# Kernel tuning notes

Measured on AMD Instinct MI355X. Metric: run time of the kernel, lower is better.

## Reference

```python
import jax, jax.numpy as jnp
import numpy as np

B, NS, NT = 4, 512, 512
D_IN, C1, R, C2 = 128, 64, 32, 32
E = 32768
STEPS = 10


def setup_inputs() -> dict:
    key = jax.random.key(0)
    ks = jax.random.split(key, 12)
    inp = {}
    inp['x_s'] = jax.random.normal(ks[0], (B * NS, D_IN), jnp.float32)
    inp['edge_index_s'] = jax.random.randint(ks[1], (2, E), 0, B * NS, jnp.int32)
    inp['edge_attr_s'] = jax.random.uniform(ks[2], (E,), jnp.float32)
    inp['batch_s'] = (jnp.arange(B * NS, dtype=jnp.int32) // NS)
    inp['x_t'] = jax.random.normal(ks[3], (B * NT, D_IN), jnp.float32)
    inp['edge_index_t'] = jax.random.randint(ks[4], (2, E), 0, B * NT, jnp.int32)
    inp['edge_attr_t'] = jax.random.uniform(ks[5], (E,), jnp.float32)
    inp['batch_t'] = (jnp.arange(B * NT, dtype=jnp.int32) // NT)
    inp['W1'] = jax.random.normal(ks[6], (D_IN, C1), jnp.float32) / np.float32(np.sqrt(D_IN))
    inp['W2'] = jax.random.normal(ks[7], (R, C2), jnp.float32) / np.float32(np.sqrt(R))
    inp['mw1'] = jax.random.normal(ks[8], (C2, C2), jnp.float32) / np.float32(np.sqrt(C2))
    inp['mb1'] = jnp.zeros((C2,), jnp.float32)
    inp['mw2'] = jax.random.normal(ks[9], (C2, 1), jnp.float32) / np.float32(np.sqrt(C2))
    inp['mb2'] = jnp.zeros((1,), jnp.float32)
    inp['r'] = jax.random.normal(ks[10], (STEPS, B, NS, R), jnp.float32)
    return inp


def psi(x, src, dst, ea, W, n):
    # simple message-passing GNN: edge-weighted neighbor aggregation + linear + ReLU
    m = jax.ops.segment_sum(x[src] * ea[:, None], dst, num_segments=n)
    return jax.nn.relu((x + m) @ W)


def reference(x_s, edge_index_s, edge_attr_s, batch_s, x_t, edge_index_t, edge_attr_t,
              batch_t, W1, W2, mw1, mb1, mw2, mb2, r):
    # Uniform graph sizes -> to_dense_batch is a reshape and all masks are True,
    # so masked_softmax reduces to plain softmax; batch_s/batch_t kept for interface fidelity.
    ss, ds = edge_index_s[0], edge_index_s[1]
    st, dt = edge_index_t[0], edge_index_t[1]
    h_s = psi(x_s, ss, ds, edge_attr_s, W1, B * NS).reshape(B, NS, C1)
    h_t = psi(x_t, st, dt, edge_attr_t, W1, B * NT).reshape(B, NT, C1)
    S_hat0 = jnp.einsum('bsc,btc->bst', h_s, h_t)  # [B, NS, NT]
    S_0 = jax.nn.softmax(S_hat0, axis=-1)

    def step(S_hat, r_i):
        S = jax.nn.softmax(S_hat, axis=-1)
        r_t = jnp.einsum('bst,bsr->btr', S, r_i)  # S^T @ r_s
        o_s = psi(r_i.reshape(B * NS, R), ss, ds, edge_attr_s, W2, B * NS).reshape(B, NS, C2)
        o_t = psi(r_t.reshape(B * NT, R), st, dt, edge_attr_t, W2, B * NT).reshape(B, NT, C2)
        Dm = o_s[:, :, None, :] - o_t[:, None, :, :]  # [B, NS, NT, C2] outer difference
        upd = (jax.nn.relu(Dm @ mw1 + mb1) @ mw2 + mb2)[..., 0]
        return S_hat + upd, None

    S_hat, _ = jax.lax.scan(step, S_hat0, r)
    S_L = jax.nn.softmax(S_hat, axis=-1)
    return (S_0, S_L)
```

## Files before the change

kernel.cpp:

```cpp
#include <hip/hip_runtime.h>


constexpr int kB = 4;
constexpr int kNS = 512;
constexpr int kNT = 512;
constexpr int kDin = 128;
constexpr int kC1 = 64;
constexpr int kR = 32;
constexpr int kC2 = 32;
constexpr int kE = 32768;
constexpr int kSteps = 10;
constexpr int kN = kB * kNS;
constexpr int kChunkStride = kR * kN;

__global__ void k_hist(const int* __restrict__ ei_s, const int* __restrict__ ei_t,
                       int* __restrict__ deg) {
  int g = blockIdx.y;
  const int* dst = (g ? ei_t : ei_s) + kE;
  int e = blockIdx.x * 256 + threadIdx.x;
  atomicAdd(&deg[g * kN + dst[e]], 1);
}

__global__ void k_scan(const int* __restrict__ deg, int* __restrict__ off,
                       int* __restrict__ cur) {
  int g = blockIdx.x;
  const int* d = deg + g * kN;
  int* o = off + g * (kN + 1);
  int* c = cur + g * kN;
  __shared__ int sums[256];
  int tid = threadIdx.x;
  int loc[8];
  int s = 0;
#pragma unroll
  for (int i = 0; i < 8; ++i) { loc[i] = d[tid * 8 + i]; s += loc[i]; }
  sums[tid] = s;
  __syncthreads();
  for (int st = 1; st < 256; st <<= 1) {
    int v = (tid >= st) ? sums[tid - st] : 0;
    __syncthreads();
    sums[tid] += v;
    __syncthreads();
  }
  int base = (tid > 0) ? sums[tid - 1] : 0;
#pragma unroll
  for (int i = 0; i < 8; ++i) {
    int idx = tid * 8 + i;
    o[idx] = base;
    c[idx] = base;
    base += loc[i];
  }
  if (tid == 255) o[kN] = base;
}

__global__ void k_scatter(const int* __restrict__ ei_s, const int* __restrict__ ei_t,
                          const float* __restrict__ ea_s, const float* __restrict__ ea_t,
                          int* __restrict__ cur, int* __restrict__ srcs,
                          float* __restrict__ eaw) {
  int g = blockIdx.y;
  const int* ei = g ? ei_t : ei_s;
  const float* ea = g ? ea_t : ea_s;
  int e = blockIdx.x * 256 + threadIdx.x;
  int d = ei[kE + e];
  int srcv = ei[e];
  int pos = atomicAdd(&cur[g * kN + d], 1);
  srcs[g * kE + pos] = srcv;
  eaw[g * kE + pos] = ea[e];
}

__global__ __launch_bounds__(128) void k_psi1(
    const float* __restrict__ x_s, const float* __restrict__ x_t,
    const int* __restrict__ srcs, const float* __restrict__ eaw,
    const int* __restrict__ off, const float* __restrict__ W1, float* __restrict__ h) {
  int g = blockIdx.y;
  const float* x = g ? x_t : x_s;
  const int* sr = srcs + g * kE;
  const float* ew = eaw + g * kE;
  const int* o = off + g * (kN + 1);
  float* ho = h + (size_t)g * kN * kC1;
  int n = blockIdx.x, f = threadIdx.x;
  __shared__ float y[kDin];
  int beg = o[n], end = o[n + 1];
  float m = 0.f;
  for (int idx = beg; idx < end; ++idx)
    m += x[(size_t)sr[idx] * kDin + f] * ew[idx];
  y[f] = x[(size_t)n * kDin + f] + m;
  __syncthreads();
  if (f < kC1) {
    float acc = 0.f;
#pragma unroll 16
    for (int k = 0; k < kDin; ++k) acc += y[k] * W1[k * kC1 + f];
    ho[(size_t)n * kC1 + f] = fmaxf(acc, 0.f);
  }
}

__global__ __launch_bounds__(256) void k_shat0(const float* __restrict__ h,
                                               float* __restrict__ Shat,
                                               float* __restrict__ pstatm,
                                               float* __restrict__ pstatl) {
  int b = blockIdx.z, s0 = blockIdx.y * 64, t0 = blockIdx.x * 64;
  const float* hs = h + (size_t)(b * kNS + s0) * kC1;
  const float* ht = h + (size_t)kN * kC1 + (size_t)(b * kNT + t0) * kC1;
  __shared__ float As[64 * 68];
  __shared__ float Bs[64 * 68];
  int tid = threadIdx.x;
#pragma unroll
  for (int k2 = 0; k2 < 4; ++k2) {
    int idx = tid + k2 * 256;
    int row = idx >> 4, c4 = idx & 15;
    float4 va = *(const float4*)(hs + (size_t)row * kC1 + c4 * 4);
    *(float4*)&As[row * 68 + c4 * 4] = va;
    float4 vb = *(const float4*)(ht + (size_t)row * kC1 + c4 * 4);
    *(float4*)&Bs[row * 68 + c4 * 4] = vb;
  }
  __syncthreads();
  int ts = tid >> 4, tt = tid & 15;
  float acc[4][4] = {};
#pragma unroll
  for (int cc = 0; cc < 16; ++cc) {
    float4 a[4], bt[4];
#pragma unroll
    for (int i = 0; i < 4; ++i) a[i] = *(const float4*)&As[(ts * 4 + i) * 68 + cc * 4];
#pragma unroll
    for (int k = 0; k < 4; ++k) bt[k] = *(const float4*)&Bs[(tt + 16 * k) * 68 + cc * 4];
#pragma unroll
    for (int i = 0; i < 4; ++i)
#pragma unroll
      for (int k = 0; k < 4; ++k)
        acc[i][k] += a[i].x * bt[k].x + a[i].y * bt[k].y + a[i].z * bt[k].z + a[i].w * bt[k].w;
  }
#pragma unroll
  for (int i = 0; i < 4; ++i) {
    int s = s0 + ts * 4 + i;
    float* row = Shat + (size_t)(b * kNS + s) * kNT;
#pragma unroll
    for (int k = 0; k < 4; ++k) row[t0 + tt + 16 * k] = acc[i][k];
  }
#pragma unroll
  for (int i = 0; i < 4; ++i) {
    float mm = fmaxf(fmaxf(acc[i][0], acc[i][1]), fmaxf(acc[i][2], acc[i][3]));
#pragma unroll
    for (int o2 = 8; o2; o2 >>= 1) mm = fmaxf(mm, __shfl_xor(mm, o2, 64));
    float se = 0.f;
#pragma unroll
    for (int k = 0; k < 4; ++k) se += __expf(acc[i][k] - mm);
#pragma unroll
    for (int o2 = 8; o2; o2 >>= 1) se += __shfl_xor(se, o2, 64);
    if (tt == 0) {
      int grow = b * kNS + s0 + ts * 4 + i;
      pstatm[blockIdx.x * kN + grow] = mm;
      pstatl[blockIdx.x * kN + grow] = se;
    }
  }
}

__global__ __launch_bounds__(256) void k_rt(const float* __restrict__ Shat,
                                            const float* __restrict__ pstatm,
                                            const float* __restrict__ pstatl,
                                            const float* __restrict__ ri,
                                            float* __restrict__ part, int nc,
                                            float* __restrict__ Sout) {
  int b = blockIdx.z, cs = blockIdx.y, s0 = cs * 64, t0 = blockIdx.x * 64;
  __shared__ float Wt[64 * 64];
  __shared__ float rch[64 * 32];
  __shared__ float lm[64], ll[64];
  int tid = threadIdx.x;
  if (tid < 64) {
    int row = b * kNS + s0 + tid;
    float m = -3.4e38f;
    for (int c = 0; c < nc; ++c) m = fmaxf(m, pstatm[c * kN + row]);
    float l = 0.f;
    for (int c = 0; c < nc; ++c) l += __expf(pstatm[c * kN + row] - m) * pstatl[c * kN + row];
    lm[tid] = m;
    ll[tid] = 1.f / l;
  }
  __syncthreads();
#pragma unroll
  for (int k2 = 0; k2 < 4; ++k2) {
    int idx = tid + k2 * 256;
    int row = idx >> 4, c4 = idx & 15;
    int grow = b * kNS + s0 + row;
    float4 v = *(const float4*)(Shat + (size_t)grow * kNT + t0 + c4 * 4);
    float m = lm[row], l = ll[row];
    float4 wv;
    wv.x = __expf(v.x - m) * l;
    wv.y = __expf(v.y - m) * l;
    wv.z = __expf(v.z - m) * l;
    wv.w = __expf(v.w - m) * l;
    *(float4*)&Wt[row * 64 + c4 * 4] = wv;
    if (Sout) *(float4*)(Sout + (size_t)grow * kNT + t0 + c4 * 4) = wv;
  }
#pragma unroll
  for (int k2 = 0; k2 < 2; ++k2) {
    int idx = tid + k2 * 256;
    int row = idx >> 3, c4 = idx & 7;
    float4 v = *(const float4*)(ri + (size_t)(b * kNS + s0 + row) * kR + c4 * 4);
    *(float4*)&rch[row * 32 + c4 * 4] = v;
  }
  __syncthreads();
  int t_l = tid & 63, jg = tid >> 6;
  float acc[8] = {};
  for (int s = 0; s < 64; ++s) {
    float wv = Wt[s * 64 + t_l];
    float4 ra = *(const float4*)&rch[s * 32 + jg * 8];
    float4 rb = *(const float4*)&rch[s * 32 + jg * 8 + 4];
    acc[0] += wv * ra.x; acc[1] += wv * ra.y; acc[2] += wv * ra.z; acc[3] += wv * ra.w;
    acc[4] += wv * rb.x; acc[5] += wv * rb.y; acc[6] += wv * rb.z; acc[7] += wv * rb.w;
  }
  int gcol = b * kNT + t0 + t_l;
  float* dst = part + (size_t)cs * kChunkStride + (size_t)jg * 8 * kN + gcol;
#pragma unroll
  for (int q = 0; q < 8; ++q) dst[(size_t)q * kN] = acc[q];
}

__global__ __launch_bounds__(256) void k_red(const float* __restrict__ part,
                                             float* __restrict__ rt) {
  int idx = blockIdx.x * 256 + threadIdx.x;
  int j = idx >> 11, col = idx & (kN - 1);
  float s = 0.f;
#pragma unroll
  for (int cs = 0; cs < 8; ++cs) s += part[(size_t)cs * kChunkStride + idx];
  rt[(size_t)col * kR + j] = s;
}

__device__ __forceinline__ void psi2_node(
    int n, const float* __restrict__ vin, const int* __restrict__ sr,
    const float* __restrict__ ew, const int* __restrict__ o,
    const float* __restrict__ W2, const float* __restrict__ mw1,
    const float* __restrict__ mb1, float* __restrict__ Pout) {
  int lane = threadIdx.x & 63;
  int f = lane & 31, hh = lane >> 5;
  int beg = o[n], end = o[n + 1];
  float m = 0.f;
  for (int idx = beg + hh; idx < end; idx += 2)
    m += vin[(size_t)sr[idx] * kR + f] * ew[idx];
  m += __shfl_down(m, 32, 64);
  float v = vin[(size_t)n * kR + f] + m;
  float acc = 0.f;
#pragma unroll
  for (int k = 0; k < kC2; ++k) acc += __shfl(v, k, 64) * W2[k * kC2 + f];
  float ov = fmaxf(acc, 0.f);
  float p = mb1 ? mb1[f] : 0.f;
#pragma unroll
  for (int k = 0; k < kC2; ++k) p += __shfl(ov, k, 64) * mw1[k * kC2 + f];
  if (lane < 32) Pout[(size_t)n * kC2 + f] = p;
}

__global__ __launch_bounds__(256) void k_psi2s(
    const float* __restrict__ r, const int* __restrict__ srcs,
    const float* __restrict__ eaw, const int* __restrict__ off,
    const float* __restrict__ W2, const float* __restrict__ mw1,
    const float* __restrict__ mb1, float* __restrict__ PsAll) {
  int nn = blockIdx.x * 4 + (threadIdx.x >> 6);
  int step = nn >> 11, node = nn & (kN - 1);
  psi2_node(node, r + (size_t)step * kN * kR, srcs, eaw, off, W2, mw1, mb1,
            PsAll + (size_t)step * kN * kR);
}

__global__ __launch_bounds__(256) void k_psi2t(
    const float* __restrict__ rt, const int* __restrict__ srcs,
    const float* __restrict__ eaw, const int* __restrict__ off,
    const float* __restrict__ W2, const float* __restrict__ mw1,
    float* __restrict__ Pt) {
  int n = blockIdx.x * 4 + (threadIdx.x >> 6);
  psi2_node(n, rt, srcs + kE, eaw + kE, off + (kN + 1), W2, mw1, nullptr, Pt);
}

__global__ __launch_bounds__(256) void k_upd(
    float* __restrict__ Shat, const float* __restrict__ Ps,
    const float* __restrict__ Pt, const float* __restrict__ mw2,
    const float* __restrict__ mb2, float* __restrict__ pstatm,
    float* __restrict__ pstatl) {
  __shared__ float pts[256 * 33];
  __shared__ float red[8 * 4];
  __shared__ float lmx[8];
  int tid = threadIdx.x;
  int g0 = blockIdx.x * 8;
  int cc = blockIdx.y;
  int bb = g0 >> 9;
  int c0 = cc * 256;
  const float4* PtB = (const float4*)(Pt + ((size_t)bb * kNT + c0) * kC2);
#pragma unroll
  for (int k = 0; k < 8; ++k) {
    int idx = tid + k * 256;
    int col = idx >> 3, q = idx & 7;
    float4 v = PtB[idx];
    float* d = &pts[col * 33 + q * 4];
    d[0] = v.x; d[1] = v.y; d[2] = v.z; d[3] = v.w;
  }
  __syncthreads();
  float pt[32];
#pragma unroll
  for (int j = 0; j < 32; ++j) pt[j] = pts[tid * 33 + j];
  float bias = mb2[0];
  float nv[8];
#pragma unroll
  for (int s = 0; s < 8; ++s) {
    const float* psr = Ps + (size_t)(g0 + s) * kC2;
    float u = 0.f;
#pragma unroll
    for (int j = 0; j < 32; ++j) u += fmaxf(psr[j] - pt[j], 0.f) * mw2[j];
    float* p = Shat + (size_t)(g0 + s) * kNT + c0 + tid;
    float v = *p + u + bias;
    *p = v;
    nv[s] = v;
  }
  int wv = tid >> 6, ln = tid & 63;
#pragma unroll
  for (int s = 0; s < 8; ++s) {
    float m = nv[s];
#pragma unroll
    for (int o2 = 32; o2; o2 >>= 1) m = fmaxf(m, __shfl_down(m, o2, 64));
    if (ln == 0) red[s * 4 + wv] = m;
  }
  __syncthreads();
  if (tid < 8) {
    lmx[tid] = fmaxf(fmaxf(red[tid * 4], red[tid * 4 + 1]),
                     fmaxf(red[tid * 4 + 2], red[tid * 4 + 3]));
  }
  __syncthreads();
#pragma unroll
  for (int s = 0; s < 8; ++s) {
    float e = __expf(nv[s] - lmx[s]);
#pragma unroll
    for (int o2 = 32; o2; o2 >>= 1) e += __shfl_down(e, o2, 64);
    if (ln == 0) red[s * 4 + wv] = e;
  }
  __syncthreads();
  if (tid < 8) {
    float l = red[tid * 4] + red[tid * 4 + 1] + red[tid * 4 + 2] + red[tid * 4 + 3];
    pstatm[cc * kN + g0 + tid] = lmx[tid];
    pstatl[cc * kN + g0 + tid] = l;
  }
}

__global__ __launch_bounds__(256) void k_out(const float* __restrict__ Shat,
                                             const float* __restrict__ pstatm,
                                             const float* __restrict__ pstatl,
                                             float* __restrict__ out) {
  int row = blockIdx.x, tid = threadIdx.x;
  float m0 = pstatm[row], m1 = pstatm[kN + row];
  float l0 = pstatl[row], l1 = pstatl[kN + row];
  float m = fmaxf(m0, m1);
  float linv = 1.f / (__expf(m0 - m) * l0 + __expf(m1 - m) * l1);
  const float* p = Shat + (size_t)row * kNT;
  float* d = out + (size_t)row * kNT;
  d[tid] = __expf(p[tid] - m) * linv;
  d[tid + 256] = __expf(p[tid + 256] - m) * linv;
}

extern "C" void kernel_launch(void* const* d_in, const int* in_sizes, int n_in,
                              void* d_out, int out_size, void* d_ws, size_t ws_size,
                              hipStream_t stream) {
  (void)in_sizes; (void)n_in; (void)out_size; (void)ws_size;
  const float* x_s = (const float*)d_in[0];
  const int* ei_s = (const int*)d_in[1];
  const float* ea_s = (const float*)d_in[2];
  const float* x_t = (const float*)d_in[4];
  const int* ei_t = (const int*)d_in[5];
  const float* ea_t = (const float*)d_in[6];
  const float* W1 = (const float*)d_in[8];
  const float* W2 = (const float*)d_in[9];
  const float* mw1 = (const float*)d_in[10];
  const float* mb1 = (const float*)d_in[11];
  const float* mw2 = (const float*)d_in[12];
  const float* mb2 = (const float*)d_in[13];
  const float* r = (const float*)d_in[14];
  float* out = (float*)d_out;

  char* w = (char*)d_ws;
  auto alloc = [&](size_t bytes) -> void* {
    void* p = (void*)w;
    w += (bytes + 255) & ~(size_t)255;
    return p;
  };
  int* deg = (int*)alloc((size_t)2 * kN * 4);
  int* off = (int*)alloc((size_t)2 * (kN + 1) * 4);
  int* cur = (int*)alloc((size_t)2 * kN * 4);
  int* srcs = (int*)alloc((size_t)2 * kE * 4);
  float* eaw = (float*)alloc((size_t)2 * kE * 4);
  float* h = (float*)alloc((size_t)2 * kN * kC1 * 4);
  float* Shat = (float*)alloc((size_t)kB * kNS * kNT * 4);
  float* pstatm = (float*)alloc((size_t)8 * kN * 4);
  float* pstatl = (float*)alloc((size_t)8 * kN * 4);
  float* rt = (float*)alloc((size_t)kN * kR * 4);
  float* PsAll = (float*)alloc((size_t)kSteps * kN * kR * 4);
  float* Pt = (float*)alloc((size_t)kN * kC2 * 4);
  float* part = (float*)alloc((size_t)8 * kChunkStride * 4);

  hipMemsetAsync(deg, 0, (size_t)2 * kN * 4, stream);
  k_hist<<<dim3(kE / 256, 2), 256, 0, stream>>>(ei_s, ei_t, deg);
  k_scan<<<2, 256, 0, stream>>>(deg, off, cur);
  k_scatter<<<dim3(kE / 256, 2), 256, 0, stream>>>(ei_s, ei_t, ea_s, ea_t, cur, srcs, eaw);
  k_psi2s<<<kSteps * kN / 4, 256, 0, stream>>>(r, srcs, eaw, off, W2, mw1, mb1, PsAll);
  k_psi1<<<dim3(kN, 2), 128, 0, stream>>>(x_s, x_t, srcs, eaw, off, W1, h);
  k_shat0<<<dim3(8, 8, kB), 256, 0, stream>>>(h, Shat, pstatm, pstatl);
  k_rt<<<dim3(8, 8, kB), 256, 0, stream>>>(Shat, pstatm, pstatl, r, part, 8, out);
  k_red<<<kChunkStride / 256, 256, 0, stream>>>(part, rt);
  for (int i = 0; i < kSteps; ++i) {
    k_psi2t<<<kN / 4, 256, 0, stream>>>(rt, srcs, eaw, off, W2, mw1, Pt);
    k_upd<<<dim3(kN / 8, 2), 256, 0, stream>>>(Shat, PsAll + (size_t)i * kN * kR, Pt,
                                               mw2, mb2, pstatm, pstatl);
    if (i + 1 < kSteps) {
      k_rt<<<dim3(8, 8, kB), 256, 0, stream>>>(Shat, pstatm, pstatl,
                                               r + (size_t)(i + 1) * kN * kR, part,
                                               2, nullptr);
      k_red<<<kChunkStride / 256, 256, 0, stream>>>(part, rt);
    }
  }
  k_out<<<kN, 256, 0, stream>>>(Shat, pstatm, pstatl, out + (size_t)kB * kNS * kNT);
}
```

Before: 486.4 us.

## Fuse CSR build into one block kernel, merge psi1/psi2s, pad segments

```diff
diff --git a/kernel.cpp b/kernel.cpp
--- a/kernel.cpp
+++ b/kernel.cpp
@@ -11,85 +11,122 @@
 constexpr int kE = 32768;
 constexpr int kSteps = 10;
 constexpr int kN = kB * kNS;
+constexpr int kEP = kE + 8 * kN;
 constexpr int kChunkStride = kR * kN;
 
-__global__ void k_hist(const int* __restrict__ ei_s, const int* __restrict__ ei_t,
-                       int* __restrict__ deg) {
-  int g = blockIdx.y;
-  const int* dst = (g ? ei_t : ei_s) + kE;
-  int e = blockIdx.x * 256 + threadIdx.x;
-  atomicAdd(&deg[g * kN + dst[e]], 1);
-}
-
-__global__ void k_scan(const int* __restrict__ deg, int* __restrict__ off,
-                       int* __restrict__ cur) {
+__global__ __launch_bounds__(1024) void k_csr(
+    const int* __restrict__ ei_s, const float* __restrict__ ea_s,
+    const int* __restrict__ ei_t, const float* __restrict__ ea_t,
+    int* __restrict__ off, int* __restrict__ srcs, float* __restrict__ eaw) {
   int g = blockIdx.x;
-  const int* d = deg + g * kN;
+  const int* ei = g ? ei_t : ei_s;
+  const float* ea = g ? ea_t : ea_s;
   int* o = off + g * (kN + 1);
-  int* c = cur + g * kN;
-  __shared__ int sums[256];
+  int* sg = srcs + g * kEP;
+  float* eg = eaw + g * kEP;
+  __shared__ int cnt[kN];
+  __shared__ int base[kN];
+  __shared__ int sums[1024];
   int tid = threadIdx.x;
-  int loc[8];
-  int s = 0;
-#pragma unroll
-  for (int i = 0; i < 8; ++i) { loc[i] = d[tid * 8 + i]; s += loc[i]; }
-  sums[tid] = s;
-  __syncthreads();
-  for (int st = 1; st < 256; st <<= 1) {
+  cnt[tid] = 0;
+  cnt[tid + 1024] = 0;
+  __syncthreads();
+  for (int e = tid; e < kE; e += 1024) atomicAdd(&cnt[ei[kE + e]], 1);
+  __syncthreads();
+  int c0 = (cnt[2 * tid] + 7) & ~7;
+  int c1 = (cnt[2 * tid + 1] + 7) & ~7;
+  sums[tid] = c0 + c1;
+  __syncthreads();
+  for (int st = 1; st < 1024; st <<= 1) {
     int v = (tid >= st) ? sums[tid - st] : 0;
     __syncthreads();
     sums[tid] += v;
     __syncthreads();
   }
-  int base = (tid > 0) ? sums[tid - 1] : 0;
-#pragma unroll
-  for (int i = 0; i < 8; ++i) {
-    int idx = tid * 8 + i;
-    o[idx] = base;
-    c[idx] = base;
-    base += loc[i];
-  }
-  if (tid == 255) o[kN] = base;
-}
-
-__global__ void k_scatter(const int* __restrict__ ei_s, const int* __restrict__ ei_t,
-                          const float* __restrict__ ea_s, const float* __restrict__ ea_t,
-                          int* __restrict__ cur, int* __restrict__ srcs,
-                          float* __restrict__ eaw) {
-  int g = blockIdx.y;
-  const int* ei = g ? ei_t : ei_s;
-  const float* ea = g ? ea_t : ea_s;
-  int e = blockIdx.x * 256 + threadIdx.x;
-  int d = ei[kE + e];
-  int srcv = ei[e];
-  int pos = atomicAdd(&cur[g * kN + d], 1);
-  srcs[g * kE + pos] = srcv;
-  eaw[g * kE + pos] = ea[e];
-}
-
-__global__ __launch_bounds__(128) void k_psi1(
-    const float* __restrict__ x_s, const float* __restrict__ x_t,
-    const int* __restrict__ srcs, const float* __restrict__ eaw,
-    const int* __restrict__ off, const float* __restrict__ W1, float* __restrict__ h) {
-  int g = blockIdx.y;
-  const float* x = g ? x_t : x_s;
-  const int* sr = srcs + g * kE;
-  const float* ew = eaw + g * kE;
-  const int* o = off + g * (kN + 1);
-  float* ho = h + (size_t)g * kN * kC1;
-  int n = blockIdx.x, f = threadIdx.x;
-  __shared__ float y[kDin];
+  int b = (tid > 0) ? sums[tid - 1] : 0;
+  base[2 * tid] = b;
+  base[2 * tid + 1] = b + c0;
+  o[2 * tid] = b;
+  o[2 * tid + 1] = b + c0;
+  if (tid == 1023) o[kN] = sums[1023];
+  __syncthreads();
+#pragma unroll
+  for (int h2 = 0; h2 < 2; ++h2) {
+    int n = 2 * tid + h2;
+    int bs = base[n], c = cnt[n], pc = (c + 7) & ~7;
+    for (int k = bs + c; k < bs + pc; ++k) { sg[k] = 0; eg[k] = 0.f; }
+  }
+  __syncthreads();
+  for (int e = tid; e < kE; e += 1024) {
+    int d = ei[kE + e];
+    int pos = atomicAdd(&base[d], 1);
+    sg[pos] = ei[e];
+    eg[pos] = ea[e];
+  }
+}
+
+__device__ __forceinline__ void psi2_node(
+    int n, const float* __restrict__ vin, const int* __restrict__ sr,
+    const float* __restrict__ ew, const int* __restrict__ o,
+    const float* __restrict__ W2, const float* __restrict__ mw1,
+    const float* __restrict__ mb1, float* __restrict__ Pout) {
+  int lane = threadIdx.x & 63;
+  int f = lane & 31, hh = lane >> 5;
   int beg = o[n], end = o[n + 1];
   float m = 0.f;
-  for (int idx = beg; idx < end; ++idx)
-    m += x[(size_t)sr[idx] * kDin + f] * ew[idx];
-  y[f] = x[(size_t)n * kDin + f] + m;
-  __syncthreads();
-  if (f < kC1) {
-    float acc = 0.f;
+  for (int b0 = beg + hh * 4; b0 < end; b0 += 8) {
+#pragma unroll
+    for (int q = 0; q < 4; ++q)
+      m += vin[(size_t)sr[b0 + q] * kR + f] * ew[b0 + q];
+  }
+  m += __shfl_down(m, 32, 64);
+  float v = vin[(size_t)n * kR + f] + m;
+  float acc = 0.f;
+#pragma unroll
+  for (int k = 0; k < kC2; ++k) acc += __shfl(v, k, 64) * W2[k * kC2 + f];
+  float ov = fmaxf(acc, 0.f);
+  float p = mb1 ? mb1[f] : 0.f;
+#pragma unroll
+  for (int k = 0; k < kC2; ++k) p += __shfl(ov, k, 64) * mw1[k * kC2 + f];
+  if (lane < 32) Pout[(size_t)n * kC2 + f] = p;
+}
+
+__global__ __launch_bounds__(256) void k_pre(
+    const float* __restrict__ x_s, const float* __restrict__ x_t,
+    const float* __restrict__ r, const int* __restrict__ srcs,
+    const float* __restrict__ eaw, const int* __restrict__ off,
+    const float* __restrict__ W1, const float* __restrict__ W2,
+    const float* __restrict__ mw1, const float* __restrict__ mb1,
+    float* __restrict__ h, float* __restrict__ PsAll) {
+  int bid = blockIdx.x, tid = threadIdx.x;
+  if (bid < 2048) {
+    int g = bid >> 10;
+    int n = (bid & 1023) * 2 + (tid >> 7);
+    int f = tid & 127;
+    const float* x = g ? x_t : x_s;
+    const int* sr = srcs + g * kEP;
+    const float* ew = eaw + g * kEP;
+    const int* o = off + g * (kN + 1);
+    float* ho = h + (size_t)g * kN * kC1;
+    __shared__ float y[2][kDin];
+    int beg = o[n], end = o[n + 1];
+    float m = 0.f;
+    for (int idx = beg; idx < end; ++idx)
+      m += x[(size_t)sr[idx] * kDin + f] * ew[idx];
+    y[tid >> 7][f] = x[(size_t)n * kDin + f] + m;
+    __syncthreads();
+    if (f < kC1) {
+      const float* yy = y[tid >> 7];
+      float acc = 0.f;
 #pragma unroll 16
-    for (int k = 0; k < kDin; ++k) acc += y[k] * W1[k * kC1 + f];
-    ho[(size_t)n * kC1 + f] = fmaxf(acc, 0.f);
+      for (int k = 0; k < kDin; ++k) acc += yy[k] * W1[k * kC1 + f];
+      ho[(size_t)n * kC1 + f] = fmaxf(acc, 0.f);
+    }
+  } else {
+    int nn = (bid - 2048) * 4 + (tid >> 6);
+    int step = nn >> 11, node = nn & (kN - 1);
+    psi2_node(node, r + (size_t)step * kN * kR, srcs, eaw, off, W2, mw1, mb1,
+              PsAll + (size_t)step * kN * kR);
   }
 }
 
@@ -222,47 +259,13 @@
   rt[(size_t)col * kR + j] = s;
 }
 
-__device__ __forceinline__ void psi2_node(
-    int n, const float* __restrict__ vin, const int* __restrict__ sr,
-    const float* __restrict__ ew, const int* __restrict__ o,
-    const float* __restrict__ W2, const float* __restrict__ mw1,
-    const float* __restrict__ mb1, float* __restrict__ Pout) {
-  int lane = threadIdx.x & 63;
-  int f = lane & 31, hh = lane >> 5;
-  int beg = o[n], end = o[n + 1];
-  float m = 0.f;
-  for (int idx = beg + hh; idx < end; idx += 2)
-    m += vin[(size_t)sr[idx] * kR + f] * ew[idx];
-  m += __shfl_down(m, 32, 64);
-  float v = vin[(size_t)n * kR + f] + m;
-  float acc = 0.f;
-#pragma unroll
-  for (int k = 0; k < kC2; ++k) acc += __shfl(v, k, 64) * W2[k * kC2 + f];
-  float ov = fmaxf(acc, 0.f);
-  float p = mb1 ? mb1[f] : 0.f;
-#pragma unroll
-  for (int k = 0; k < kC2; ++k) p += __shfl(ov, k, 64) * mw1[k * kC2 + f];
-  if (lane < 32) Pout[(size_t)n * kC2 + f] = p;
-}
-
-__global__ __launch_bounds__(256) void k_psi2s(
-    const float* __restrict__ r, const int* __restrict__ srcs,
-    const float* __restrict__ eaw, const int* __restrict__ off,
-    const float* __restrict__ W2, const float* __restrict__ mw1,
-    const float* __restrict__ mb1, float* __restrict__ PsAll) {
-  int nn = blockIdx.x * 4 + (threadIdx.x >> 6);
-  int step = nn >> 11, node = nn & (kN - 1);
-  psi2_node(node, r + (size_t)step * kN * kR, srcs, eaw, off, W2, mw1, mb1,
-            PsAll + (size_t)step * kN * kR);
-}
-
 __global__ __launch_bounds__(256) void k_psi2t(
     const float* __restrict__ rt, const int* __restrict__ srcs,
     const float* __restrict__ eaw, const int* __restrict__ off,
     const float* __restrict__ W2, const float* __restrict__ mw1,
     float* __restrict__ Pt) {
   int n = blockIdx.x * 4 + (threadIdx.x >> 6);
-  psi2_node(n, rt, srcs + kE, eaw + kE, off + (kN + 1), W2, mw1, nullptr, Pt);
+  psi2_node(n, rt, srcs + kEP, eaw + kEP, off + (kN + 1), W2, mw1, nullptr, Pt);
 }
 
 __global__ __launch_bounds__(256) void k_upd(
@@ -287,6 +290,9 @@
     float* d = &pts[col * 33 + q * 4];
     d[0] = v.x; d[1] = v.y; d[2] = v.z; d[3] = v.w;
   }
+  float old[8];
+#pragma unroll
+  for (int s = 0; s < 8; ++s) old[s] = Shat[(size_t)(g0 + s) * kNT + c0 + tid];
   __syncthreads();
   float pt[32];
 #pragma unroll
@@ -299,9 +305,8 @@
     float u = 0.f;
 #pragma unroll
     for (int j = 0; j < 32; ++j) u += fmaxf(psr[j] - pt[j], 0.f) * mw2[j];
-    float* p = Shat + (size_t)(g0 + s) * kNT + c0 + tid;
-    float v = *p + u + bias;
-    *p = v;
+    float v = old[s] + u + bias;
+    Shat[(size_t)(g0 + s) * kNT + c0 + tid] = v;
     nv[s] = v;
   }
   int wv = tid >> 6, ln = tid & 63;
@@ -373,11 +378,9 @@
     w += (bytes + 255) & ~(size_t)255;
     return p;
   };
-  int* deg = (int*)alloc((size_t)2 * kN * 4);
   int* off = (int*)alloc((size_t)2 * (kN + 1) * 4);
-  int* cur = (int*)alloc((size_t)2 * kN * 4);
-  int* srcs = (int*)alloc((size_t)2 * kE * 4);
-  float* eaw = (float*)alloc((size_t)2 * kE * 4);
+  int* srcs = (int*)alloc((size_t)2 * kEP * 4);
+  float* eaw = (float*)alloc((size_t)2 * kEP * 4);
   float* h = (float*)alloc((size_t)2 * kN * kC1 * 4);
   float* Shat = (float*)alloc((size_t)kB * kNS * kNT * 4);
   float* pstatm = (float*)alloc((size_t)8 * kN * 4);
@@ -387,12 +390,9 @@
   float* Pt = (float*)alloc((size_t)kN * kC2 * 4);
   float* part = (float*)alloc((size_t)8 * kChunkStride * 4);
 
-  hipMemsetAsync(deg, 0, (size_t)2 * kN * 4, stream);
-  k_hist<<<dim3(kE / 256, 2), 256, 0, stream>>>(ei_s, ei_t, deg);
-  k_scan<<<2, 256, 0, stream>>>(deg, off, cur);
-  k_scatter<<<dim3(kE / 256, 2), 256, 0, stream>>>(ei_s, ei_t, ea_s, ea_t, cur, srcs, eaw);
-  k_psi2s<<<kSteps * kN / 4, 256, 0, stream>>>(r, srcs, eaw, off, W2, mw1, mb1, PsAll);
-  k_psi1<<<dim3(kN, 2), 128, 0, stream>>>(x_s, x_t, srcs, eaw, off, W1, h);
+  k_csr<<<2, 1024, 0, stream>>>(ei_s, ea_s, ei_t, ea_t, off, srcs, eaw);
+  k_pre<<<7168, 256, 0, stream>>>(x_s, x_t, r, srcs, eaw, off, W1, W2, mw1, mb1,
+                                  h, PsAll);
   k_shat0<<<dim3(8, 8, kB), 256, 0, stream>>>(h, Shat, pstatm, pstatl);
   k_rt<<<dim3(8, 8, kB), 256, 0, stream>>>(Shat, pstatm, pstatl, r, part, 8, out);
   k_red<<<kChunkStride / 256, 256, 0, stream>>>(part, rt);
```

Measured after the change: 515.1 us. 1.06x slower.

## Pad CSR rows to multiples of eight and fuse psi1 with psi2s precompute

Applied to the files above, without the earlier changes.

```diff
diff --git a/kernel.cpp b/kernel.cpp
--- a/kernel.cpp
+++ b/kernel.cpp
@@ -11,6 +11,7 @@
 constexpr int kE = 32768;
 constexpr int kSteps = 10;
 constexpr int kN = kB * kNS;
+constexpr int kEP = kE + 8 * kN;
 constexpr int kChunkStride = kR * kN;
 
 __global__ void k_hist(const int* __restrict__ ei_s, const int* __restrict__ ei_t,
@@ -32,7 +33,10 @@
   int loc[8];
   int s = 0;
 #pragma unroll
-  for (int i = 0; i < 8; ++i) { loc[i] = d[tid * 8 + i]; s += loc[i]; }
+  for (int i = 0; i < 8; ++i) {
+    loc[i] = (d[tid * 8 + i] + 7) & ~7;
+    s += loc[i];
+  }
   sums[tid] = s;
   __syncthreads();
   for (int st = 1; st < 256; st <<= 1) {
@@ -63,33 +67,75 @@
   int d = ei[kE + e];
   int srcv = ei[e];
   int pos = atomicAdd(&cur[g * kN + d], 1);
-  srcs[g * kE + pos] = srcv;
-  eaw[g * kE + pos] = ea[e];
-}
-
-__global__ __launch_bounds__(128) void k_psi1(
-    const float* __restrict__ x_s, const float* __restrict__ x_t,
-    const int* __restrict__ srcs, const float* __restrict__ eaw,
-    const int* __restrict__ off, const float* __restrict__ W1, float* __restrict__ h) {
-  int g = blockIdx.y;
-  const float* x = g ? x_t : x_s;
-  const int* sr = srcs + g * kE;
-  const float* ew = eaw + g * kE;
-  const int* o = off + g * (kN + 1);
-  float* ho = h + (size_t)g * kN * kC1;
-  int n = blockIdx.x, f = threadIdx.x;
-  __shared__ float y[kDin];
+  srcs[g * kEP + pos] = srcv;
+  eaw[g * kEP + pos] = ea[e];
+}
+
+__device__ __forceinline__ void psi2_node(
+    int n, const float* __restrict__ vin, const int* __restrict__ sr,
+    const float* __restrict__ ew, const int* __restrict__ o,
+    const float* __restrict__ W2, const float* __restrict__ mw1,
+    const float* __restrict__ mb1, float* __restrict__ Pout) {
+  int lane = threadIdx.x & 63;
+  int f = lane & 31, hh = lane >> 5;
   int beg = o[n], end = o[n + 1];
   float m = 0.f;
-  for (int idx = beg; idx < end; ++idx)
-    m += x[(size_t)sr[idx] * kDin + f] * ew[idx];
-  y[f] = x[(size_t)n * kDin + f] + m;
-  __syncthreads();
-  if (f < kC1) {
-    float acc = 0.f;
+  for (int b0 = beg + hh * 4; b0 < end; b0 += 8) {
+#pragma unroll
+    for (int q = 0; q < 4; ++q)
+      m += vin[(size_t)sr[b0 + q] * kR + f] * ew[b0 + q];
+  }
+  m += __shfl_down(m, 32, 64);
+  float v = vin[(size_t)n * kR + f] + m;
+  float acc = 0.f;
+#pragma unroll
+  for (int k = 0; k < kC2; ++k) acc += __shfl(v, k, 64) * W2[k * kC2 + f];
+  float ov = fmaxf(acc, 0.f);
+  float p = mb1 ? mb1[f] : 0.f;
+#pragma unroll
+  for (int k = 0; k < kC2; ++k) p += __shfl(ov, k, 64) * mw1[k * kC2 + f];
+  if (lane < 32) Pout[(size_t)n * kC2 + f] = p;
+}
+
+__global__ __launch_bounds__(256) void k_pre(
+    const float* __restrict__ x_s, const float* __restrict__ x_t,
+    const float* __restrict__ r, const int* __restrict__ srcs,
+    const float* __restrict__ eaw, const int* __restrict__ off,
+    const float* __restrict__ W1, const float* __restrict__ W2,
+    const float* __restrict__ mw1, const float* __restrict__ mb1,
+    float* __restrict__ h, float* __restrict__ PsAll) {
+  int bid = blockIdx.x, tid = threadIdx.x;
+  if (bid < 2048) {
+    int g = bid >> 10;
+    int n = (bid & 1023) * 2 + (tid >> 7);
+    int f = tid & 127;
+    const float* x = g ? x_t : x_s;
+    const int* sr = srcs + g * kEP;
+    const float* ew = eaw + g * kEP;
+    const int* o = off + g * (kN + 1);
+    float* ho = h + (size_t)g * kN * kC1;
+    __shared__ float y[2][kDin];
+    int beg = o[n], end = o[n + 1];
+    float m = 0.f;
+    for (int idx = beg; idx < end; idx += 2) {
+      float m2 = x[(size_t)sr[idx + 1] * kDin + f] * ew[idx + 1];
+      m += x[(size_t)sr[idx] * kDin + f] * ew[idx];
+      m += m2;
+    }
+    y[tid >> 7][f] = x[(size_t)n * kDin + f] + m;
+    __syncthreads();
+    if (f < kC1) {
+      const float* yy = y[tid >> 7];
+      float acc = 0.f;
 #pragma unroll 16
-    for (int k = 0; k < kDin; ++k) acc += y[k] * W1[k * kC1 + f];
-    ho[(size_t)n * kC1 + f] = fmaxf(acc, 0.f);
+      for (int k = 0; k < kDin; ++k) acc += yy[k] * W1[k * kC1 + f];
+      ho[(size_t)n * kC1 + f] = fmaxf(acc, 0.f);
+    }
+  } else {
+    int nn = (bid - 2048) * 4 + (tid >> 6);
+    int step = nn >> 11, node = nn & (kN - 1);
+    psi2_node(node, r + (size_t)step * kN * kR, srcs, eaw, off, W2, mw1, mb1,
+              PsAll + (size_t)step * kN * kR);
   }
 }
 
@@ -222,47 +268,13 @@
   rt[(size_t)col * kR + j] = s;
 }
 
-__device__ __forceinline__ void psi2_node(
-    int n, const float* __restrict__ vin, const int* __restrict__ sr,
-    const float* __restrict__ ew, const int* __restrict__ o,
-    const float* __restrict__ W2, const float* __restrict__ mw1,
-    const float* __restrict__ mb1, float* __restrict__ Pout) {
-  int lane = threadIdx.x & 63;
-  int f = lane & 31, hh = lane >> 5;
-  int beg = o[n], end = o[n + 1];
-  float m = 0.f;
-  for (int idx = beg + hh; idx < end; idx += 2)
-    m += vin[(size_t)sr[idx] * kR + f] * ew[idx];
-  m += __shfl_down(m, 32, 64);
-  float v = vin[(size_t)n * kR + f] + m;
-  float acc = 0.f;
-#pragma unroll
-  for (int k = 0; k < kC2; ++k) acc += __shfl(v, k, 64) * W2[k * kC2 + f];
-  float ov = fmaxf(acc, 0.f);
-  float p = mb1 ? mb1[f] : 0.f;
-#pragma unroll
-  for (int k = 0; k < kC2; ++k) p += __shfl(ov, k, 64) * mw1[k * kC2 + f];
-  if (lane < 32) Pout[(size_t)n * kC2 + f] = p;
-}
-
-__global__ __launch_bounds__(256) void k_psi2s(
-    const float* __restrict__ r, const int* __restrict__ srcs,
-    const float* __restrict__ eaw, const int* __restrict__ off,
-    const float* __restrict__ W2, const float* __restrict__ mw1,
-    const float* __restrict__ mb1, float* __restrict__ PsAll) {
-  int nn = blockIdx.x * 4 + (threadIdx.x >> 6);
-  int step = nn >> 11, node = nn & (kN - 1);
-  psi2_node(node, r + (size_t)step * kN * kR, srcs, eaw, off, W2, mw1, mb1,
-            PsAll + (size_t)step * kN * kR);
-}
-
 __global__ __launch_bounds__(256) void k_psi2t(
     const float* __restrict__ rt, const int* __restrict__ srcs,
     const float* __restrict__ eaw, const int* __restrict__ off,
     const float* __restrict__ W2, const float* __restrict__ mw1,
     float* __restrict__ Pt) {
   int n = blockIdx.x * 4 + (threadIdx.x >> 6);
-  psi2_node(n, rt, srcs + kE, eaw + kE, off + (kN + 1), W2, mw1, nullptr, Pt);
+  psi2_node(n, rt, srcs + kEP, eaw + kEP, off + (kN + 1), W2, mw1, nullptr, Pt);
 }
 
 __global__ __launch_bounds__(256) void k_upd(
@@ -287,6 +299,9 @@
     float* d = &pts[col * 33 + q * 4];
     d[0] = v.x; d[1] = v.y; d[2] = v.z; d[3] = v.w;
   }
+  float old[8];
+#pragma unroll
+  for (int s = 0; s < 8; ++s) old[s] = Shat[(size_t)(g0 + s) * kNT + c0 + tid];
   __syncthreads();
   float pt[32];
 #pragma unroll
@@ -299,9 +314,8 @@
     float u = 0.f;
 #pragma unroll
     for (int j = 0; j < 32; ++j) u += fmaxf(psr[j] - pt[j], 0.f) * mw2[j];
-    float* p = Shat + (size_t)(g0 + s) * kNT + c0 + tid;
-    float v = *p + u + bias;
-    *p = v;
+    float v = old[s] + u + bias;
+    Shat[(size_t)(g0 + s) * kNT + c0 + tid] = v;
     nv[s] = v;
   }
   int wv = tid >> 6, ln = tid & 63;
@@ -374,10 +388,11 @@
     return p;
   };
   int* deg = (int*)alloc((size_t)2 * kN * 4);
+  int* cur = (int*)alloc((size_t)2 * kN * 4);
+  int* srcs = (int*)alloc((size_t)2 * kEP * 4);
+  float* eaw = (float*)alloc((size_t)2 * kEP * 4);
+  size_t zbytes = (size_t)((char*)(eaw + 2 * kEP) - (char*)deg);
   int* off = (int*)alloc((size_t)2 * (kN + 1) * 4);
-  int* cur = (int*)alloc((size_t)2 * kN * 4);
-  int* srcs = (int*)alloc((size_t)2 * kE * 4);
-  float* eaw = (float*)alloc((size_t)2 * kE * 4);
   float* h = (float*)alloc((size_t)2 * kN * kC1 * 4);
   float* Shat = (float*)alloc((size_t)kB * kNS * kNT * 4);
   float* pstatm = (float*)alloc((size_t)8 * kN * 4);
@@ -387,12 +402,12 @@
   float* Pt = (float*)alloc((size_t)kN * kC2 * 4);
   float* part = (float*)alloc((size_t)8 * kChunkStride * 4);
 
-  hipMemsetAsync(deg, 0, (size_t)2 * kN * 4, stream);
+  hipMemsetAsync(deg, 0, zbytes, stream);
   k_hist<<<dim3(kE / 256, 2), 256, 0, stream>>>(ei_s, ei_t, deg);
   k_scan<<<2, 256, 0, stream>>>(deg, off, cur);
   k_scatter<<<dim3(kE / 256, 2), 256, 0, stream>>>(ei_s, ei_t, ea_s, ea_t, cur, srcs, eaw);
-  k_psi2s<<<kSteps * kN / 4, 256, 0, stream>>>(r, srcs, eaw, off, W2, mw1, mb1, PsAll);
-  k_psi1<<<dim3(kN, 2), 128, 0, stream>>>(x_s, x_t, srcs, eaw, off, W1, h);
+  k_pre<<<7168, 256, 0, stream>>>(x_s, x_t, r, srcs, eaw, off, W1, W2, mw1, mb1,
+                                  h, PsAll);
   k_shat0<<<dim3(8, 8, kB), 256, 0, stream>>>(h, Shat, pstatm, pstatl);
   k_rt<<<dim3(8, 8, kB), 256, 0, stream>>>(Shat, pstatm, pstatl, r, part, 8, out);
   k_red<<<kChunkStride / 256, 256, 0, stream>>>(part, rt);
```

After: 445.9 us. 1.09x faster.
